# Kernel tuning notes

Measured on AMD Instinct MI355X. Metric: run time of the kernel, lower is better.

Reference implementation:

```python
import jax, jax.numpy as jnp
import numpy as np

DILATION = 512
C_RES = 128
C_SKIP = 256


def setup_inputs() -> dict:
    key = jax.random.key(0)
    ks = jax.random.split(key, 6)
    B, T = 8, 16384
    x = jax.random.normal(ks[0], (B, C_RES, T), dtype=jnp.float32)
    # dilated conv weight: [out_ch, in_ch, kernel=2], no bias
    w_dil = jax.random.normal(ks[1], (C_RES, C_RES, 2), dtype=jnp.float32) * (1.0 / np.sqrt(2 * C_RES))
    # 1x1 residual conv (with bias)
    w_res = jax.random.normal(ks[2], (C_RES, C_RES), dtype=jnp.float32) * (1.0 / np.sqrt(C_RES))
    b_res = jax.random.normal(ks[3], (C_RES,), dtype=jnp.float32) * 0.01
    # 1x1 skip conv (with bias)
    w_skip = jax.random.normal(ks[4], (C_SKIP, C_RES), dtype=jnp.float32) * (1.0 / np.sqrt(C_RES))
    b_skip = jax.random.normal(ks[5], (C_SKIP,), dtype=jnp.float32) * 0.01
    return {"x": x, "w_dil": w_dil, "w_res": w_res, "b_res": b_res,
            "w_skip": w_skip, "b_skip": b_skip, "skip_size": 4096}


def reference(x, w_dil, w_res, b_res, w_skip, b_skip, skip_size):
    # x: [B, C, T]. Dilated causal conv, kernel_size=2, dilation=DILATION, no padding:
    # pre[:, :, t] = W[:,:,0] @ x[:,:,t] + W[:,:,1] @ x[:,:,t+DILATION], t in [0, T-DILATION)
    T = x.shape[2]
    L = T - DILATION  # output length
    pre = (jnp.einsum('oi,bit->bot', w_dil[:, :, 0], x[:, :, :L]) +
           jnp.einsum('oi,bit->bot', w_dil[:, :, 1], x[:, :, DILATION:]))
    activated = jnp.tanh(pre) * jax.nn.sigmoid(pre)  # filter * gate
    # 1x1 residual conv + residual add with the time-aligned tail of x
    out = (jnp.einsum('oi,bit->bot', w_res, activated) + b_res[None, :, None]
           + x[:, :, T - L:])
    # 1x1 skip conv, keep last skip_size steps
    skip = jnp.einsum('oi,bit->bot', w_skip, activated) + b_skip[None, :, None]
    skip = skip[:, :, -skip_size:]
    return (out, skip)
```

## Files before the change

### kernel.cpp

```cpp
#include <hip/hip_runtime.h>

typedef float f32x4 __attribute__((ext_vector_type(4)));
typedef __bf16 bf16x8 __attribute__((ext_vector_type(8)));

__device__ __forceinline__ unsigned short f2bf(float f) {
  unsigned u = __builtin_bit_cast(unsigned, f);
  u = (u + 0x7FFFu + ((u >> 16) & 1u)) >> 16;
  return (unsigned short)u;
}

__device__ __forceinline__ f32x4 MFMA16(uint4 a, uint4 b, f32x4 c) {
  return __builtin_amdgcn_mfma_f32_16x16x32_bf16(
      __builtin_bit_cast(bf16x8, a), __builtin_bit_cast(bf16x8, b), c, 0, 0, 0);
}

__global__ void wn_prep(const float* __restrict__ wd, const float* __restrict__ wres,
                        const float* __restrict__ wskip, unsigned short* __restrict__ ws16) {
  int g = blockIdx.x * 256 + threadIdx.x;
  if (g < 40960) {
    int kc = g / 5120, rem = g - kc * 5120;
    int o = rem / 40, c = rem - o * 40;
    float v = 0.f;
    if (c < 32) {
      int k = kc * 32 + c;
      int tap = k >> 7, i = k & 127;
      v = wd[(o << 8) + (i << 1) + tap];
    }
    ws16[g] = f2bf(v);
  } else {
    int g2 = g - 40960;
    int p = g2 / 17408, rem = g2 - p * 17408;
    int r = rem / 136, c = rem - r * 136;
    float v = 0.f;
    if (c < 128) {
      if (p == 0) v = wres[(r << 7) + c];
      else        v = wskip[(((p - 1) << 7) + r) * 128 + c];
    }
    ws16[40960 + g2] = f2bf(v);
  }
}

__global__ __launch_bounds__(512, 4) void wn_main(
    const float* __restrict__ x,
    const float* __restrict__ bres_g,
    const float* __restrict__ bskip_g,
    const unsigned short* __restrict__ wd_img,
    const unsigned short* __restrict__ wrs_img,
    float* __restrict__ out,
    float* __restrict__ skipo) {
  extern __shared__ unsigned short lds[];
  unsigned short* xls  = lds;
  unsigned short* wls  = lds + 10240;
  unsigned short* actT = lds + 20480;
  unsigned short* wrsb = lds;

  const int tile = blockIdx.x;
  const int b = blockIdx.y;
  const int t0 = tile * 128;
  const int tid = threadIdx.x;
  const int lane = tid & 63;
  const int wv = tid >> 6;
  const int mw = wv >> 2;
  const int nw = wv & 3;
  const int l15 = lane & 15;
  const int lhi = lane >> 4;

  const int kq = tid & 7;
  const int tpr = tid >> 3;

  const float* xb_base = x + (size_t)b * (128 * 16384);

  float2 xr[3][4];
  uint4  wr0[3];
  unsigned wr1[3];

  auto issueChunk = [&](int c) {
    int s = c % 3;
    int kglob = c * 32 + kq * 4;
    int tap = kglob >> 7;
    int ib = kglob & 127;
    const float* p = xb_base + (size_t)ib * 16384 + (t0 + tap * 512 + tpr * 2);
    xr[s][0] = *(const float2*)(p);
    xr[s][1] = *(const float2*)(p + 16384);
    xr[s][2] = *(const float2*)(p + 32768);
    xr[s][3] = *(const float2*)(p + 49152);
    wr0[s] = ((const uint4*)(wd_img + c * 5120))[tid];
    wr1[s] = ((const unsigned*)(wd_img + c * 5120))[2048 + tid];
  };
  auto writeChunk = [&](int c, int buf) {
    int s = c % 3;
    unsigned short* dst = xls + buf * 5120;
    int r0 = tpr * 2;
    ushort4 a0, a1;
    a0.x = f2bf(xr[s][0].x); a0.y = f2bf(xr[s][1].x); a0.z = f2bf(xr[s][2].x); a0.w = f2bf(xr[s][3].x);
    a1.x = f2bf(xr[s][0].y); a1.y = f2bf(xr[s][1].y); a1.z = f2bf(xr[s][2].y); a1.w = f2bf(xr[s][3].y);
    *(ushort4*)(dst + r0 * 40 + kq * 4) = a0;
    *(ushort4*)(dst + (r0 + 1) * 40 + kq * 4) = a1;
    unsigned short* wdst = wls + buf * 5120;
    ((uint4*)wdst)[tid] = wr0[s];
    ((unsigned*)wdst)[2048 + tid] = wr1[s];
  };

  f32x4 acc[4][2];
#pragma unroll
  for (int i = 0; i < 4; ++i)
#pragma unroll
    for (int j = 0; j < 2; ++j) acc[i][j] = (f32x4){0.f, 0.f, 0.f, 0.f};

  issueChunk(0); issueChunk(1); issueChunk(2);
  writeChunk(0, 0);
  __syncthreads();

#pragma unroll
  for (int kc = 0; kc < 8; ++kc) {
    const int buf = kc & 1;
    if (kc + 3 < 8) issueChunk(kc + 3);
    const unsigned short* wb = wls + buf * 5120;
    const unsigned short* xb = xls + buf * 5120;
    uint4 af[4], bfr[2];
#pragma unroll
    for (int mi = 0; mi < 4; ++mi)
      af[mi] = *(const uint4*)(wb + (mw * 64 + mi * 16 + l15) * 40 + lhi * 8);
#pragma unroll
    for (int ni = 0; ni < 2; ++ni)
      bfr[ni] = *(const uint4*)(xb + (nw * 32 + ni * 16 + l15) * 40 + lhi * 8);
#pragma unroll
    for (int mi = 0; mi < 4; ++mi)
#pragma unroll
      for (int ni = 0; ni < 2; ++ni)
        acc[mi][ni] = MFMA16(af[mi], bfr[ni], acc[mi][ni]);
    if (kc < 7) writeChunk(kc + 1, buf ^ 1);
    __syncthreads();
  }

#pragma unroll
  for (int mi = 0; mi < 4; ++mi) {
#pragma unroll
    for (int ni = 0; ni < 2; ++ni) {
      ushort4 av;
#pragma unroll
      for (int r = 0; r < 4; ++r) {
        float p = acc[mi][ni][r];
        p = fminf(fmaxf(p, -15.f), 15.f);
        float ep = __expf(p);
        float e2 = ep * ep;
        float sg = ep * __builtin_amdgcn_rcpf(1.f + ep);
        float th = (e2 - 1.f) * __builtin_amdgcn_rcpf(e2 + 1.f);
        ((unsigned short*)&av)[r] = f2bf(th * sg);
      }
      int trow = nw * 32 + ni * 16 + l15;
      int o0 = mw * 64 + mi * 16 + lhi * 4;
      *(ushort4*)(actT + trow * 136 + o0) = av;
    }
  }

  const int npass = (tile >= 92) ? 3 : 1;
  for (int p = 0; p < npass; ++p) {
    {
      const uint4* src = (const uint4*)(wrs_img + p * 17408);
      uint4* dst = (uint4*)wrsb;
      dst[tid] = src[tid];
      dst[tid + 512] = src[tid + 512];
      dst[tid + 1024] = src[tid + 1024];
      dst[tid + 1536] = src[tid + 1536];
      if (tid < 128) dst[tid + 2048] = src[tid + 2048];
    }
    __syncthreads();

    f32x4 acc2[4][2];
#pragma unroll
    for (int i = 0; i < 4; ++i)
#pragma unroll
      for (int j = 0; j < 2; ++j) acc2[i][j] = (f32x4){0.f, 0.f, 0.f, 0.f};

#pragma unroll
    for (int kk = 0; kk < 4; ++kk) {
      uint4 af[4], bfr[2];
#pragma unroll
      for (int mi = 0; mi < 4; ++mi)
        af[mi] = *(const uint4*)(wrsb + (mw * 64 + mi * 16 + l15) * 136 + kk * 32 + lhi * 8);
#pragma unroll
      for (int ni = 0; ni < 2; ++ni)
        bfr[ni] = *(const uint4*)(actT + (nw * 32 + ni * 16 + l15) * 136 + kk * 32 + lhi * 8);
#pragma unroll
      for (int mi = 0; mi < 4; ++mi)
#pragma unroll
        for (int ni = 0; ni < 2; ++ni)
          acc2[mi][ni] = MFMA16(af[mi], bfr[ni], acc2[mi][ni]);
    }

    if (p == 0) {
#pragma unroll
      for (int mi = 0; mi < 4; ++mi) {
        int o0 = mw * 64 + mi * 16 + lhi * 4;
        float br[4];
#pragma unroll
        for (int r = 0; r < 4; ++r) br[r] = bres_g[o0 + r];
#pragma unroll
        for (int ni = 0; ni < 2; ++ni) {
          int tl = nw * 32 + ni * 16 + l15;
#pragma unroll
          for (int r = 0; r < 4; ++r) {
            size_t row = (size_t)(b * 128 + o0 + r);
            float v = acc2[mi][ni][r] + br[r] + x[row * 16384 + 512 + t0 + tl];
            out[row * 15872 + t0 + tl] = v;
          }
        }
      }
    } else {
#pragma unroll
      for (int mi = 0; mi < 4; ++mi) {
        int o2 = (p - 1) * 128 + mw * 64 + mi * 16 + lhi * 4;
        float bs[4];
#pragma unroll
        for (int r = 0; r < 4; ++r) bs[r] = bskip_g[o2 + r];
#pragma unroll
        for (int ni = 0; ni < 2; ++ni) {
          int tl = nw * 32 + ni * 16 + l15;
          int s = t0 + tl - 11776;
#pragma unroll
          for (int r = 0; r < 4; ++r) {
            skipo[(size_t)(b * 256 + o2 + r) * 4096 + s] = acc2[mi][ni][r] + bs[r];
          }
        }
      }
    }
    __syncthreads();
  }
}

extern "C" void kernel_launch(void* const* d_in, const int* in_sizes, int n_in,
                              void* d_out, int out_size, void* d_ws, size_t ws_size,
                              hipStream_t stream) {
  const float* x      = (const float*)d_in[0];
  const float* w_dil  = (const float*)d_in[1];
  const float* w_res  = (const float*)d_in[2];
  const float* b_res  = (const float*)d_in[3];
  const float* w_skip = (const float*)d_in[4];
  const float* b_skip = (const float*)d_in[5];
  unsigned short* ws16 = (unsigned short*)d_ws;
  float* out = (float*)d_out;
  float* skipo = out + 16252928;

  wn_prep<<<364, 256, 0, stream>>>(w_dil, w_res, w_skip, ws16);

  dim3 grid(124, 8);
  wn_main<<<grid, 512, 75776, stream>>>(x, b_res, b_skip, ws16, ws16 + 40960, out, skipo);
}
```

Measured before the change: 91.77 us.

## Read weight fragments directly from global memory, shrink LDS, use LDS-only barriers

The dilated-conv and residual/skip weight fragments are now loaded straight from global/L2 into registers for the MFMA A operands instead of being staged through LDS. This cuts LDS use per block, which together with the higher launch-bounds occupancy hint lets more blocks fit per CU. The x register prefetch depth drops from three chunks to two. Barriers now wait only on LDS counters and skip draining global loads, so prefetches can stay in flight across sync points. In exchange, every wave issues redundant global weight loads, adding L2/L1 traffic and latency that the extra occupancy has to hide.

```diff
diff --git a/kernel.cpp b/kernel.cpp
--- a/kernel.cpp
+++ b/kernel.cpp
@@ -12,6 +12,12 @@
 __device__ __forceinline__ f32x4 MFMA16(uint4 a, uint4 b, f32x4 c) {
   return __builtin_amdgcn_mfma_f32_16x16x32_bf16(
       __builtin_bit_cast(bf16x8, a), __builtin_bit_cast(bf16x8, b), c, 0, 0, 0);
+}
+
+__device__ __forceinline__ void barrier_noglobal() {
+  asm volatile("s_waitcnt lgkmcnt(0)" ::: "memory");
+  __builtin_amdgcn_s_barrier();
+  asm volatile("" ::: "memory");
 }
 
 __global__ void wn_prep(const float* __restrict__ wd, const float* __restrict__ wres,
@@ -40,7 +46,7 @@
   }
 }
 
-__global__ __launch_bounds__(512, 4) void wn_main(
+__global__ __launch_bounds__(512, 6) void wn_main(
     const float* __restrict__ x,
     const float* __restrict__ bres_g,
     const float* __restrict__ bskip_g,
@@ -50,9 +56,7 @@
     float* __restrict__ skipo) {
   extern __shared__ unsigned short lds[];
   unsigned short* xls  = lds;
-  unsigned short* wls  = lds + 10240;
-  unsigned short* actT = lds + 20480;
-  unsigned short* wrsb = lds;
+  unsigned short* actT = lds;
 
   const int tile = blockIdx.x;
   const int b = blockIdx.y;
@@ -70,12 +74,10 @@
 
   const float* xb_base = x + (size_t)b * (128 * 16384);
 
-  float2 xr[3][4];
-  uint4  wr0[3];
-  unsigned wr1[3];
-
-  auto issueChunk = [&](int c) {
-    int s = c % 3;
+  float2 xr[2][4];
+
+  auto issueX = [&](int c) {
+    int s = c & 1;
     int kglob = c * 32 + kq * 4;
     int tap = kglob >> 7;
     int ib = kglob & 127;
@@ -84,11 +86,9 @@
     xr[s][1] = *(const float2*)(p + 16384);
     xr[s][2] = *(const float2*)(p + 32768);
     xr[s][3] = *(const float2*)(p + 49152);
-    wr0[s] = ((const uint4*)(wd_img + c * 5120))[tid];
-    wr1[s] = ((const unsigned*)(wd_img + c * 5120))[2048 + tid];
   };
-  auto writeChunk = [&](int c, int buf) {
-    int s = c % 3;
+  auto writeX = [&](int c, int buf) {
+    int s = c & 1;
     unsigned short* dst = xls + buf * 5120;
     int r0 = tpr * 2;
     ushort4 a0, a1;
@@ -96,9 +96,6 @@
     a1.x = f2bf(xr[s][0].y); a1.y = f2bf(xr[s][1].y); a1.z = f2bf(xr[s][2].y); a1.w = f2bf(xr[s][3].y);
     *(ushort4*)(dst + r0 * 40 + kq * 4) = a0;
     *(ushort4*)(dst + (r0 + 1) * 40 + kq * 4) = a1;
-    unsigned short* wdst = wls + buf * 5120;
-    ((uint4*)wdst)[tid] = wr0[s];
-    ((unsigned*)wdst)[2048 + tid] = wr1[s];
   };
 
   f32x4 acc[4][2];
@@ -107,20 +104,20 @@
 #pragma unroll
     for (int j = 0; j < 2; ++j) acc[i][j] = (f32x4){0.f, 0.f, 0.f, 0.f};
 
-  issueChunk(0); issueChunk(1); issueChunk(2);
-  writeChunk(0, 0);
-  __syncthreads();
+  issueX(0); issueX(1);
+  writeX(0, 0);
+  barrier_noglobal();
 
 #pragma unroll
   for (int kc = 0; kc < 8; ++kc) {
     const int buf = kc & 1;
-    if (kc + 3 < 8) issueChunk(kc + 3);
-    const unsigned short* wb = wls + buf * 5120;
+    uint4 af[4];
+#pragma unroll
+    for (int mi = 0; mi < 4; ++mi)
+      af[mi] = *(const uint4*)(wd_img + kc * 5120 + (mw * 64 + mi * 16 + l15) * 40 + lhi * 8);
+    if (kc + 2 < 8) issueX(kc + 2);
+    uint4 bfr[2];
     const unsigned short* xb = xls + buf * 5120;
-    uint4 af[4], bfr[2];
-#pragma unroll
-    for (int mi = 0; mi < 4; ++mi)
-      af[mi] = *(const uint4*)(wb + (mw * 64 + mi * 16 + l15) * 40 + lhi * 8);
 #pragma unroll
     for (int ni = 0; ni < 2; ++ni)
       bfr[ni] = *(const uint4*)(xb + (nw * 32 + ni * 16 + l15) * 40 + lhi * 8);
@@ -129,8 +126,8 @@
 #pragma unroll
       for (int ni = 0; ni < 2; ++ni)
         acc[mi][ni] = MFMA16(af[mi], bfr[ni], acc[mi][ni]);
-    if (kc < 7) writeChunk(kc + 1, buf ^ 1);
-    __syncthreads();
+    if (kc < 7) writeX(kc + 1, buf ^ 1);
+    barrier_noglobal();
   }
 
 #pragma unroll
@@ -153,20 +150,10 @@
       *(ushort4*)(actT + trow * 136 + o0) = av;
     }
   }
+  barrier_noglobal();
 
   const int npass = (tile >= 92) ? 3 : 1;
   for (int p = 0; p < npass; ++p) {
-    {
-      const uint4* src = (const uint4*)(wrs_img + p * 17408);
-      uint4* dst = (uint4*)wrsb;
-      dst[tid] = src[tid];
-      dst[tid + 512] = src[tid + 512];
-      dst[tid + 1024] = src[tid + 1024];
-      dst[tid + 1536] = src[tid + 1536];
-      if (tid < 128) dst[tid + 2048] = src[tid + 2048];
-    }
-    __syncthreads();
-
     f32x4 acc2[4][2];
 #pragma unroll
     for (int i = 0; i < 4; ++i)
@@ -178,7 +165,7 @@
       uint4 af[4], bfr[2];
 #pragma unroll
       for (int mi = 0; mi < 4; ++mi)
-        af[mi] = *(const uint4*)(wrsb + (mw * 64 + mi * 16 + l15) * 136 + kk * 32 + lhi * 8);
+        af[mi] = *(const uint4*)(wrs_img + p * 17408 + (mw * 64 + mi * 16 + l15) * 136 + kk * 32 + lhi * 8);
 #pragma unroll
       for (int ni = 0; ni < 2; ++ni)
         bfr[ni] = *(const uint4*)(actT + (nw * 32 + ni * 16 + l15) * 136 + kk * 32 + lhi * 8);
@@ -225,7 +212,6 @@
         }
       }
     }
-    __syncthreads();
   }
 }
 
@@ -245,5 +231,5 @@
   wn_prep<<<364, 256, 0, stream>>>(w_dil, w_res, w_skip, ws16);
 
   dim3 grid(124, 8);
-  wn_main<<<grid, 512, 75776, stream>>>(x, b_res, b_skip, ws16, ws16 + 40960, out, skipo);
-}
+  wn_main<<<grid, 512, 34816, stream>>>(x, b_res, b_skip, ws16, ws16 + 40960, out, skipo);
+}
```

Result: slower. 193.8 us (+111.2%).
